# Kernel optimization log

Measured on AMD Instinct MI355X. Metric: run time of the kernel, lower is better.

Reference implementation:

```python
import jax, jax.numpy as jnp
import numpy as np

V, E, H, L, B = 32004, 512, 512, 128, 64  # vocab(+4), emb, hidden, seq_len, batch


def setup_inputs() -> dict:
    key = jax.random.key(0)
    ks = jax.random.split(key, 8)
    emb = jax.random.normal(ks[0], (V, E), jnp.float32) * 0.02
    emb = emb.at[0].set(0.0)  # padding_idx = PAD = 0
    Wx_f = jax.random.normal(ks[1], (E, 3 * H), jnp.float32) * 0.05
    Wh_f = jax.random.normal(ks[2], (H, 3 * H), jnp.float32) * 0.05
    b_f = jnp.zeros((3 * H,), jnp.float32)
    Wx_b = jax.random.normal(ks[3], (E, 3 * H), jnp.float32) * 0.05
    Wh_b = jax.random.normal(ks[4], (H, 3 * H), jnp.float32) * 0.05
    b_b = jnp.zeros((3 * H,), jnp.float32)
    xs = jax.random.randint(ks[5], (L, B), 0, V)
    xs_mask = jnp.ones((L, B), jnp.float32)
    return {"xs": xs, "xs_mask": xs_mask, "emb": emb,
            "Wx_f": Wx_f, "Wh_f": Wh_f, "b_f": b_f,
            "Wx_b": Wx_b, "Wh_b": Wh_b, "b_b": b_b}


def _gru_scan(xs_e, mask, Wx, Wh, b, reverse):
    # Precompute all input-to-gate projections in one big GEMM: [L,B,3H]
    xw = jnp.einsum('lbe,eg->lbg', xs_e, Wx) + b

    def step(h, inp):
        xw_t, m = inp                       # [B,3H], [B]
        hw = h @ Wh                         # [B,3H]
        xz, xr, xh = jnp.split(xw_t, 3, -1)
        hz, hr, hh = jnp.split(hw, 3, -1)
        z = jax.nn.sigmoid(xz + hz)
        r = jax.nn.sigmoid(xr + hr)
        h_tilde = jnp.tanh(xh + r * hh)
        h_new = (1.0 - z) * h + z * h_tilde
        m = m[:, None]
        h_new = m * h_new + (1.0 - m) * h   # masked timesteps keep previous state
        return h_new, h_new

    h0 = jnp.zeros((xs_e.shape[1], Wh.shape[0]), xs_e.dtype)
    _, hs = jax.lax.scan(step, h0, (xw, mask), reverse=reverse)
    return hs  # [L,B,H], time-ordered (reverse=True already yields original order)


def reference(xs, xs_mask, emb, Wx_f, Wh_f, b_f, Wx_b, Wh_b, b_b):
    xs_e = emb[xs]                                   # [L,B,E]
    right = _gru_scan(xs_e, xs_mask, Wx_f, Wh_f, b_f, reverse=False)
    left = _gru_scan(xs_e, xs_mask, Wx_b, Wh_b, b_b, reverse=True)
    r1 = jnp.concatenate([right, left], axis=-1)      # [L,B,2H]
    r2 = left[0]                                      # final backward state (after t=0)
    return r1, r2
```

## Files before the change

kernel.cpp:

```cpp
#include <hip/hip_runtime.h>
#include <stdint.h>

typedef _Float16 f16;
typedef _Float16 f16x8 __attribute__((ext_vector_type(8)));
typedef float    f32x4 __attribute__((ext_vector_type(4)));
typedef unsigned long long u64;

#define L_    128
#define B_    64
#define E_    512
#define H_    512
#define G3    1536
#define NCOL  3072

__device__ __forceinline__ float sigm_(float x){ return 1.0f/(1.0f + __expf(-x)); }
__device__ __forceinline__ float tanh_(float x){ return 1.0f - 2.0f/(__expf(2.0f*x) + 1.0f); }

__global__ __launch_bounds__(256) void k_zero(uint4* flags){
  flags[(size_t)blockIdx.x*256 + threadIdx.x] = make_uint4(0,0,0,0);
}

__global__ __launch_bounds__(256) void k_embed(const int* __restrict__ xs,
                                               const float* __restrict__ emb,
                                               f16* __restrict__ Xe){
  int row = blockIdx.x*2 + (threadIdx.x >> 7);
  int c   = (threadIdx.x & 127) * 4;
  int idx = xs[row];
  float4 v = *(const float4*)(emb + (size_t)idx*E_ + c);
  union { f16 h[4]; uint2 u; } p;
  p.h[0] = (f16)v.x; p.h[1] = (f16)v.y; p.h[2] = (f16)v.z; p.h[3] = (f16)v.w;
  *(uint2*)(Xe + (size_t)row*E_ + c) = p.u;
}

__global__ __launch_bounds__(256) void k_transpose(const float* __restrict__ Wx_f, const float* __restrict__ Wx_b,
                                                   const float* __restrict__ Wh_f, const float* __restrict__ Wh_b,
                                                   f16* __restrict__ WxT, f16* __restrict__ WhT){
  int mat = blockIdx.z;
  const float* src = mat==0 ? Wx_f : mat==1 ? Wx_b : mat==2 ? Wh_f : Wh_b;
  f16* dst = (mat < 2) ? (WxT + (size_t)mat*G3*E_) : (WhT + (size_t)(mat-2)*G3*H_);
  int n0 = blockIdx.x*64, k0 = blockIdx.y*64;
  __shared__ f16 tile[64][65];
  int tid = threadIdx.x;
  for (int i=0;i<16;i++){
    int r = i*4 + (tid>>6);
    int c = tid & 63;
    tile[r][c] = (f16)src[(size_t)(k0+r)*G3 + n0 + c];
  }
  __syncthreads();
  for (int i=0;i<16;i++){
    int n = i*4 + (tid>>6);
    int k = tid & 63;
    dst[(size_t)(n0+n)*512 + k0 + k] = tile[k][n];
  }
}

__global__ __launch_bounds__(256) void k_gemm(const f16* __restrict__ Xe, const f16* __restrict__ WxT,
                                              const float* __restrict__ bf, const float* __restrict__ bb,
                                              f16* __restrict__ xw2){
  __shared__ __align__(16) f16 sA[128*32];
  __shared__ __align__(16) f16 sB[128*32];
  const int tid = threadIdx.x;
  const int l = tid & 63, w = tid >> 6;
  const int wr = w >> 1, wc = w & 1;
  const int m0 = blockIdx.y*128, n0 = blockIdx.x*128;
  const int rl = l & 15, sg = l >> 4;
  f32x4 acc[4][4] = {};
  for (int kk=0; kk<16; ++kk){
    __syncthreads();
    for (int i=0;i<2;i++){
      int c = i*256 + tid; int row = c>>2, s = c&3;
      int sw = s ^ ((row>>1)&3);
      *(uint4*)&sA[row*32 + sw*8] = *(const uint4*)(Xe  + (size_t)(m0+row)*512 + kk*32 + s*8);
      *(uint4*)&sB[row*32 + sw*8] = *(const uint4*)(WxT + (size_t)(n0+row)*512 + kk*32 + s*8);
    }
    __syncthreads();
    f16x8 a[4], b[4];
    for (int mi=0;mi<4;mi++){ int m=(wr*4+mi)*16+rl; a[mi] = *(const f16x8*)&sA[m*32 + ((sg^((m>>1)&3))*8)]; }
    for (int nj=0;nj<4;nj++){ int n=(wc*4+nj)*16+rl; b[nj] = *(const f16x8*)&sB[n*32 + ((sg^((n>>1)&3))*8)]; }
    for (int mi=0;mi<4;mi++)
      for (int nj=0;nj<4;nj++)
        acc[mi][nj] = __builtin_amdgcn_mfma_f32_16x16x32_f16(a[mi], b[nj], acc[mi][nj], 0,0,0);
  }
  for (int nj=0;nj<4;nj++){
    int n = n0 + (wc*4+nj)*16 + rl;
    float bias = (n < G3) ? bf[n] : bb[n-G3];
    for (int mi=0;mi<4;mi++){
      int sub = (wr*4+mi)*16 + sg*4;
      int t   = (m0 + sub) >> 6;
      int b0  = sub & 63;
      union { f16 h[4]; uint2 u; } p;
      for (int r=0;r<4;r++) p.h[r] = (f16)(acc[mi][nj][r] + bias);
      *(uint2*)(xw2 + ((size_t)t*NCOL + n)*B_ + b0) = p.u;
    }
  }
}

__global__ __launch_bounds__(256, 1) void k_scan(const f16* __restrict__ xw2, const f16* __restrict__ WhT,
                                                 f16* __restrict__ hbuf, const float* __restrict__ mask,
                                                 float* __restrict__ out, unsigned* __restrict__ flags){
  const int dir = blockIdx.x >> 5, g = blockIdx.x & 31;
  __shared__ __align__(16) f16 sW[48*512];
  __shared__ __align__(16) f16 sX[4*16*16];
  const int tid = threadIdx.x, l = tid & 63, wv = tid >> 6;
  {
    const f16* base = WhT + (size_t)dir*G3*512;
    int cs = tid & 15;
    for (int r = tid>>4; r < 48; r += 16){
      int rowg = (r>>4)*512 + g*16 + (r&15);
      const uint4* src = (const uint4*)(base + (size_t)rowg*512);
      for (int j=0;j<4;j++){
        int s = cs*4 + j;
        *(uint4*)&sW[r*512 + ((s^(r&7))*8)] = src[s];
      }
    }
  }
  const int fl = l & 15, sg = l >> 4;
  const int mb   = wv*16 + sg*4;
  const int arow = wv*16 + fl;
  const int swz  = fl & 7;
  __syncthreads();
  f16x8 pz[16], pr[16], ph[16];
  #pragma unroll
  for (int kk=0;kk<16;kk++){
    int s = kk*4 + sg;
    pz[kk] = *(const f16x8*)&sW[(     fl)*512 + ((s^swz)*8)];
    pr[kk] = *(const f16x8*)&sW[(16 + fl)*512 + ((s^swz)*8)];
    ph[kk] = *(const f16x8*)&sW[(32 + fl)*512 + ((s^swz)*8)];
  }
  #pragma unroll
  for (int kk=0;kk<16;kk++){
    asm volatile("" : "+v"(pz[kk]));
    asm volatile("" : "+v"(pr[kk]));
    asm volatile("" : "+v"(ph[kk]));
  }
  float hstate[4] = {0.f,0.f,0.f,0.f};
  float* out2 = out + (size_t)L_*B_*1024;
  unsigned* myflag = flags + (size_t)(dir*32 + g)*32;
  const unsigned* pollp = flags + (size_t)dir*1024 + (size_t)(l&31)*32;
  f16* const sXw = &sX[wv*256];
  const int prow = l >> 2, pf = (l & 3)*4;

  for (int ti=0; ti<128; ++ti){
    const int t = dir ? (127 - ti) : ti;
    size_t xb = ((size_t)t*NCOL + dir*G3 + g*16 + fl)*B_ + mb;
    union { uint2 u; f16 h[4]; } xzv, xrv, xhv;
    xzv.u = *(const uint2*)(xw2 + xb);
    xrv.u = *(const uint2*)(xw2 + xb + (size_t)512*B_);
    xhv.u = *(const uint2*)(xw2 + xb + (size_t)1024*B_);
    float4 mv4 = *(const float4*)(mask + t*B_ + mb);
    f32x4 az = {0,0,0,0}, ar = {0,0,0,0}, ah = {0,0,0,0};
    if (ti){
      unsigned tgt = (unsigned)ti;
      while (true){
        unsigned f = __hip_atomic_load(pollp, __ATOMIC_RELAXED, __HIP_MEMORY_SCOPE_AGENT);
        if (__all((int)(f >= tgt))) break;
      }
      const u64* hq = (const u64*)(hbuf + ((size_t)dir*2 + (ti&1))*(64*512)) + (size_t)arow*128;
      u64 q[32];
      #pragma unroll
      for (int kk=0;kk<16;kk++){
        int j = kk*8 + sg*2;
        q[2*kk  ] = __hip_atomic_load(hq + j,     __ATOMIC_RELAXED, __HIP_MEMORY_SCOPE_AGENT);
        q[2*kk+1] = __hip_atomic_load(hq + j + 1, __ATOMIC_RELAXED, __HIP_MEMORY_SCOPE_AGENT);
      }
      #pragma unroll
      for (int kk=0;kk<16;kk++){
        union { u64 d[2]; f16x8 h; } a;
        a.d[0] = q[2*kk]; a.d[1] = q[2*kk+1];
        az = __builtin_amdgcn_mfma_f32_16x16x32_f16(a.h, pz[kk], az, 0,0,0);
        ar = __builtin_amdgcn_mfma_f32_16x16x32_f16(a.h, pr[kk], ar, 0,0,0);
        ah = __builtin_amdgcn_mfma_f32_16x16x32_f16(a.h, ph[kk], ah, 0,0,0);
      }
    }
    #pragma unroll
    for (int r=0;r<4;r++){
      float z  = sigm_((float)xzv.h[r] + az[r]);
      float rr = sigm_((float)xrv.h[r] + ar[r]);
      float ht = tanh_((float)xhv.h[r] + rr*ah[r]);
      float mv = (&mv4.x)[r];
      float hn = (1.0f - z)*hstate[r] + z*ht;
      hn = mv*hn + (1.0f - mv)*hstate[r];
      hstate[r] = hn;
    }
    if (ti < 127){
      #pragma unroll
      for (int r=0;r<4;r++) sXw[(sg*4 + r)*16 + fl] = (f16)hstate[r];
      asm volatile("s_waitcnt lgkmcnt(0)" ::: "memory");
      u64 v = *(const u64*)&sXw[prow*16 + pf];
      f16* hb = hbuf + ((size_t)dir*2 + ((ti&1)^1))*(64*512);
      __hip_atomic_store((u64*)(hb + (size_t)(wv*16 + prow)*512 + g*16 + pf), v,
                         __ATOMIC_RELAXED, __HIP_MEMORY_SCOPE_AGENT);
      __syncthreads();
      if (tid == 0)
        __hip_atomic_store(myflag, (unsigned)(ti+1),
                           __ATOMIC_RELAXED, __HIP_MEMORY_SCOPE_AGENT);
    }
    #pragma unroll
    for (int r=0;r<4;r++){
      int m = mb + r;
      out[((size_t)(t*B_+m))*1024 + dir*512 + g*16 + fl] = hstate[r];
    }
    if (dir==1 && t==0){
      #pragma unroll
      for (int r=0;r<4;r++)
        out2[(size_t)(mb+r)*512 + g*16 + fl] = hstate[r];
    }
  }
}

extern "C" void kernel_launch(void* const* d_in, const int* in_sizes, int n_in,
                              void* d_out, int out_size, void* d_ws, size_t ws_size,
                              hipStream_t stream){
  const int*   xs      = (const int*)  d_in[0];
  const float* xs_mask = (const float*)d_in[1];
  const float* emb     = (const float*)d_in[2];
  const float* Wx_f    = (const float*)d_in[3];
  const float* Wh_f    = (const float*)d_in[4];
  const float* b_f     = (const float*)d_in[5];
  const float* Wx_b    = (const float*)d_in[6];
  const float* Wh_b    = (const float*)d_in[7];
  const float* b_b     = (const float*)d_in[8];

  char* w = (char*)d_ws;
  f16*      Xe    = (f16*)(w);
  f16*      WxT   = (f16*)(w + 8388608);
  f16*      WhT   = (f16*)(w + 11534336);
  f16*      xw2   = (f16*)(w + 14680064);
  f16*      hbuf  = (f16*)(w + 65011712);
  unsigned* flags = (unsigned*)(w + 65273856);
  float*    out   = (float*)d_out;

  k_zero     <<<dim3(2),       dim3(256), 0, stream>>>((uint4*)flags);
  k_embed    <<<dim3(4096),    dim3(256), 0, stream>>>(xs, emb, Xe);
  k_transpose<<<dim3(24,8,4),  dim3(256), 0, stream>>>(Wx_f, Wx_b, Wh_f, Wh_b, WxT, WhT);
  k_gemm     <<<dim3(24,64),   dim3(256), 0, stream>>>(Xe, WxT, b_f, b_b, xw2);
  k_scan     <<<dim3(64),      dim3(256), 0, stream>>>(xw2, WhT, hbuf, xs_mask, out, flags);
}
```

Measured before the change: 731.3 us.

## Split GRU scan into independent batch groups with smaller cross-block sync sets

The recurrent scan now splits each direction's batch into four independent 16-row groups. Each group runs on 16 blocks of 128 threads, and each block owns 32 hidden columns. Per-step flag polling and the hidden-state exchange only involve the 16 blocks of a group, and each block reads a 16-row slice of h instead of all 64 rows. This is meant to cut the latency of the per-timestep grid-wide handoff. Recurrent weights now load straight from global memory into registers without LDS staging, and the separate flag-zeroing kernel is folded into the embedding kernel to save a launch.

```diff
diff --git a/kernel.cpp b/kernel.cpp
--- a/kernel.cpp
+++ b/kernel.cpp
@@ -16,13 +16,14 @@
 __device__ __forceinline__ float sigm_(float x){ return 1.0f/(1.0f + __expf(-x)); }
 __device__ __forceinline__ float tanh_(float x){ return 1.0f - 2.0f/(__expf(2.0f*x) + 1.0f); }
 
-__global__ __launch_bounds__(256) void k_zero(uint4* flags){
-  flags[(size_t)blockIdx.x*256 + threadIdx.x] = make_uint4(0,0,0,0);
-}
-
 __global__ __launch_bounds__(256) void k_embed(const int* __restrict__ xs,
                                                const float* __restrict__ emb,
-                                               f16* __restrict__ Xe){
+                                               f16* __restrict__ Xe,
+                                               uint4* __restrict__ flags4){
+  if (blockIdx.x == 0){
+    flags4[threadIdx.x]       = make_uint4(0,0,0,0);
+    flags4[256 + threadIdx.x] = make_uint4(0,0,0,0);
+  }
   int row = blockIdx.x*2 + (threadIdx.x >> 7);
   int c   = (threadIdx.x & 127) * 4;
   int idx = xs[row];
@@ -95,37 +96,27 @@
   }
 }
 
-__global__ __launch_bounds__(256, 1) void k_scan(const f16* __restrict__ xw2, const f16* __restrict__ WhT,
+__global__ __launch_bounds__(128, 1) void k_scan(const f16* __restrict__ xw2, const f16* __restrict__ WhT,
                                                  f16* __restrict__ hbuf, const float* __restrict__ mask,
                                                  float* __restrict__ out, unsigned* __restrict__ flags){
-  const int dir = blockIdx.x >> 5, g = blockIdx.x & 31;
-  __shared__ __align__(16) f16 sW[48*512];
-  __shared__ __align__(16) f16 sX[4*16*16];
+  const int dir = blockIdx.x >> 6;
+  const int m   = (blockIdx.x >> 4) & 3;
+  const int n   = blockIdx.x & 15;
+  const int gidx = dir*4 + m;
+  __shared__ __align__(16) f16 sX[2*16*16];
   const int tid = threadIdx.x, l = tid & 63, wv = tid >> 6;
+  const int fl = l & 15, sg = l >> 4;
+  const int fbase = n*32 + wv*16;
+  f16x8 pz[16], pr[16], ph[16];
   {
-    const f16* base = WhT + (size_t)dir*G3*512;
-    int cs = tid & 15;
-    for (int r = tid>>4; r < 48; r += 16){
-      int rowg = (r>>4)*512 + g*16 + (r&15);
-      const uint4* src = (const uint4*)(base + (size_t)rowg*512);
-      for (int j=0;j<4;j++){
-        int s = cs*4 + j;
-        *(uint4*)&sW[r*512 + ((s^(r&7))*8)] = src[s];
-      }
-    }
-  }
-  const int fl = l & 15, sg = l >> 4;
-  const int mb   = wv*16 + sg*4;
-  const int arow = wv*16 + fl;
-  const int swz  = fl & 7;
-  __syncthreads();
-  f16x8 pz[16], pr[16], ph[16];
-  #pragma unroll
-  for (int kk=0;kk<16;kk++){
-    int s = kk*4 + sg;
-    pz[kk] = *(const f16x8*)&sW[(     fl)*512 + ((s^swz)*8)];
-    pr[kk] = *(const f16x8*)&sW[(16 + fl)*512 + ((s^swz)*8)];
-    ph[kk] = *(const f16x8*)&sW[(32 + fl)*512 + ((s^swz)*8)];
+    const f16* wb = WhT + (size_t)dir*G3*512;
+    #pragma unroll
+    for (int kk=0;kk<16;kk++){
+      int ko = kk*32 + sg*8;
+      pz[kk] = *(const f16x8*)(wb + (size_t)(       fbase + fl)*512 + ko);
+      pr[kk] = *(const f16x8*)(wb + (size_t)( 512 + fbase + fl)*512 + ko);
+      ph[kk] = *(const f16x8*)(wb + (size_t)(1024 + fbase + fl)*512 + ko);
+    }
   }
   #pragma unroll
   for (int kk=0;kk<16;kk++){
@@ -135,14 +126,15 @@
   }
   float hstate[4] = {0.f,0.f,0.f,0.f};
   float* out2 = out + (size_t)L_*B_*1024;
-  unsigned* myflag = flags + (size_t)(dir*32 + g)*32;
-  const unsigned* pollp = flags + (size_t)dir*1024 + (size_t)(l&31)*32;
+  const int mb = m*16 + sg*4;
+  unsigned* myflag = flags + (size_t)(n*8 + gidx)*16;
+  const unsigned* pollp = flags + (size_t)((l&15)*8 + gidx)*16;
   f16* const sXw = &sX[wv*256];
   const int prow = l >> 2, pf = (l & 3)*4;
 
   for (int ti=0; ti<128; ++ti){
     const int t = dir ? (127 - ti) : ti;
-    size_t xb = ((size_t)t*NCOL + dir*G3 + g*16 + fl)*B_ + mb;
+    size_t xb = ((size_t)t*NCOL + dir*G3 + fbase + fl)*B_ + mb;
     union { uint2 u; f16 h[4]; } xzv, xrv, xhv;
     xzv.u = *(const uint2*)(xw2 + xb);
     xrv.u = *(const uint2*)(xw2 + xb + (size_t)512*B_);
@@ -155,7 +147,7 @@
         unsigned f = __hip_atomic_load(pollp, __ATOMIC_RELAXED, __HIP_MEMORY_SCOPE_AGENT);
         if (__all((int)(f >= tgt))) break;
       }
-      const u64* hq = (const u64*)(hbuf + ((size_t)dir*2 + (ti&1))*(64*512)) + (size_t)arow*128;
+      const u64* hq = (const u64*)(hbuf + ((size_t)gidx*2 + (ti&1))*(16*512)) + (size_t)fl*128;
       u64 q[32];
       #pragma unroll
       for (int kk=0;kk<16;kk++){
@@ -187,8 +179,8 @@
       for (int r=0;r<4;r++) sXw[(sg*4 + r)*16 + fl] = (f16)hstate[r];
       asm volatile("s_waitcnt lgkmcnt(0)" ::: "memory");
       u64 v = *(const u64*)&sXw[prow*16 + pf];
-      f16* hb = hbuf + ((size_t)dir*2 + ((ti&1)^1))*(64*512);
-      __hip_atomic_store((u64*)(hb + (size_t)(wv*16 + prow)*512 + g*16 + pf), v,
+      f16* hb = hbuf + ((size_t)gidx*2 + ((ti&1)^1))*(16*512);
+      __hip_atomic_store((u64*)(hb + (size_t)prow*512 + n*32 + wv*16 + pf), v,
                          __ATOMIC_RELAXED, __HIP_MEMORY_SCOPE_AGENT);
       __syncthreads();
       if (tid == 0)
@@ -196,14 +188,12 @@
                            __ATOMIC_RELAXED, __HIP_MEMORY_SCOPE_AGENT);
     }
     #pragma unroll
-    for (int r=0;r<4;r++){
-      int m = mb + r;
-      out[((size_t)(t*B_+m))*1024 + dir*512 + g*16 + fl] = hstate[r];
-    }
+    for (int r=0;r<4;r++)
+      out[((size_t)(t*B_ + mb + r))*1024 + dir*512 + fbase + fl] = hstate[r];
     if (dir==1 && t==0){
       #pragma unroll
       for (int r=0;r<4;r++)
-        out2[(size_t)(mb+r)*512 + g*16 + fl] = hstate[r];
+        out2[(size_t)(mb + r)*512 + fbase + fl] = hstate[r];
     }
   }
 }
@@ -230,9 +220,8 @@
   unsigned* flags = (unsigned*)(w + 65273856);
   float*    out   = (float*)d_out;
 
-  k_zero     <<<dim3(2),       dim3(256), 0, stream>>>((uint4*)flags);
-  k_embed    <<<dim3(4096),    dim3(256), 0, stream>>>(xs, emb, Xe);
+  k_embed    <<<dim3(4096),    dim3(256), 0, stream>>>(xs, emb, Xe, (uint4*)flags);
   k_transpose<<<dim3(24,8,4),  dim3(256), 0, stream>>>(Wx_f, Wx_b, Wh_f, Wh_b, WxT, WhT);
   k_gemm     <<<dim3(24,64),   dim3(256), 0, stream>>>(Xe, WxT, b_f, b_b, xw2);
-  k_scan     <<<dim3(64),      dim3(256), 0, stream>>>(xw2, WhT, hbuf, xs_mask, out, flags);
-}
+  k_scan     <<<dim3(128),     dim3(128), 0, stream>>>(xw2, WhT, hbuf, xs_mask, out, flags);
+}
```

After: 613.4 us, median of 2. 1.19x faster.
